# Kernel tuning notes

Hardware: AMD Instinct MI355X
Metric: run time of the kernel (lower is better)

Reference implementation:

```python
import jax, jax.numpy as jnp
import numpy as np

T, B, I, H = 4096, 2048, 1, 10


def setup_inputs() -> dict:
    key = jax.random.key(0)
    ks = jax.random.split(key, 8)
    k = 1.0 / np.sqrt(H)  # torch default init bound for RNN and Linear(10,1)
    u = lambda kk, shape: jax.random.uniform(kk, shape, jnp.float32, -k, k)
    return {
        "x": jax.random.normal(ks[0], (T, B, I), jnp.float32),
        "h": jnp.zeros((1, B, H), jnp.float32),
        "W_ih": u(ks[1], (H, I)),
        "b_ih": u(ks[2], (H,)),
        "W_hh": u(ks[3], (H, H)),
        "b_hh": u(ks[4], (H,)),
        "W_out": u(ks[5], (1, H)),
        "b_out": u(ks[6], (1,)),
    }


def reference(x, h, W_ih, b_ih, W_hh, b_hh, W_out, b_out):
    # Vanilla RNN: h_t = tanh(x_t @ W_ih^T + b_ih + h_{t-1} @ W_hh^T + b_hh)
    b = b_ih + b_hh  # fuse the two biases once

    def step(h_prev, x_t):  # h_prev: [B,H], x_t: [B,I]
        h_new = jnp.tanh(x_t @ W_ih.T + h_prev @ W_hh.T + b)
        return h_new, h_new

    h_last, ys = jax.lax.scan(step, h[0], x)  # ys: [T,B,H]
    out = ys @ W_out.T + b_out  # [T,B,1]
    return out, h_last[None]  # h: [1,B,H]
```

## Files before the change

kernel.cpp:

```cpp
#include <hip/hip_runtime.h>

#define T_STEPS 4096
#define BATCH   2048
#define HID     10
#define UB      16

__device__ __forceinline__ void issue16(float (&xr)[UB], const float* base) {
#pragma unroll
    for (int u = 0; u < UB; ++u)
        asm volatile("global_load_dword %0, %1, off"
                     : "=v"(xr[u]) : "v"(base + (size_t)u * BATCH) : "memory");
}
#define BIND16(a) "+v"(a[0]),"+v"(a[1]),"+v"(a[2]),"+v"(a[3]),"+v"(a[4]), \
    "+v"(a[5]),"+v"(a[6]),"+v"(a[7]),"+v"(a[8]),"+v"(a[9]),"+v"(a[10]),   \
    "+v"(a[11]),"+v"(a[12]),"+v"(a[13]),"+v"(a[14]),"+v"(a[15])
__device__ __forceinline__ void wait1_bind(float (&xr)[UB]) {
    asm volatile("s_waitcnt vmcnt(1)" : BIND16(xr) :: "memory");
}
__device__ __forceinline__ void wait0_bind(float (&xr)[UB]) {
    asm volatile("s_waitcnt vmcnt(0)" : BIND16(xr) :: "memory");
}

#define STEP_HEAD \
    "v_fma_f32 %[c0], %[wih2], %[x], %[bj2]\n\t"                                    \
    "v_fmac_f32 %[c0], %[r], %[w0]\n\t"                                             \
    "v_mul_f32_dpp %[c1], %[r], %[w1] row_ror:1 row_mask:0xf bank_mask:0xf\n\t"     \
    "v_mul_f32_dpp %[c2], %[r], %[w2] row_ror:2 row_mask:0xf bank_mask:0xf\n\t"     \
    "v_fmac_f32_dpp %[c0], %[r], %[w3] row_ror:3 row_mask:0xf bank_mask:0xf\n\t"    \
    "v_fmac_f32_dpp %[c1], %[r], %[w4] row_ror:4 row_mask:0xf bank_mask:0xf\n\t"    \
    "v_fmac_f32_dpp %[c2], %[r], %[w5] row_ror:5 row_mask:0xf bank_mask:0xf\n\t"    \
    "v_fmac_f32_dpp %[c0], %[r], %[w6] row_ror:6 row_mask:0xf bank_mask:0xf\n\t"    \
    "v_fmac_f32_dpp %[c1], %[r], %[w7] row_ror:7 row_mask:0xf bank_mask:0xf\n\t"    \
    "v_fmac_f32_dpp %[c2], %[r], %[w8] row_ror:8 row_mask:0xf bank_mask:0xf\n\t"    \
    "v_fmac_f32_dpp %[c0], %[r], %[w9] row_ror:9 row_mask:0xf bank_mask:0xf\n\t"    \
    "v_fmac_f32_dpp %[c1], %[r], %[w10] row_ror:10 row_mask:0xf bank_mask:0xf\n\t"  \
    "v_fmac_f32_dpp %[c2], %[r], %[w11] row_ror:11 row_mask:0xf bank_mask:0xf\n\t"  \
    "v_fmac_f32_dpp %[c0], %[r], %[w12] row_ror:12 row_mask:0xf bank_mask:0xf\n\t"  \
    "v_fmac_f32_dpp %[c1], %[r], %[w13] row_ror:13 row_mask:0xf bank_mask:0xf\n\t"  \
    "v_fmac_f32_dpp %[c2], %[r], %[w14] row_ror:14 row_mask:0xf bank_mask:0xf\n\t"  \
    "v_fmac_f32_dpp %[c0], %[r], %[w15] row_ror:15 row_mask:0xf bank_mask:0xf\n\t"  \
    "v_add_f32 %[c1], %[c1], %[c2]\n\t"                                             \
    "v_add_f32 %[c0], %[c0], %[c1]\n\t"                                             \
    "v_exp_f32 %[ex], %[c0]\n\t"                                                    \
    "s_nop 0\n\t"                                                                   \
    "v_add_f32 %[ex], 1.0, %[ex]\n\t"

#define STEP_TAIL \
    "v_rcp_f32 %[r], %[ex]\n\t"                                                     \
    "s_nop 0"

#define PKDPP(N) "v_fmac_f32_dpp %[pk], %[c0], %[m] row_ror:" #N " row_mask:0xf bank_mask:0xf\n\t"
#define PKPLAIN  "v_fmac_f32 %[pk], %[c0], %[m]\n\t"

#define DEF_STEP(SUF, PKLINE_) \
__device__ __forceinline__ void step_##SUF(float& r, float& pk, float x, \
        float wih2, float bj2, float m, const float (&w)[16]) { \
    float c0, c1, c2, ex; \
    asm volatile( STEP_HEAD PKLINE_ STEP_TAIL \
        : [c0]"=&v"(c0), [c1]"=&v"(c1), [c2]"=&v"(c2), [ex]"=&v"(ex), \
          [r]"+v"(r), [pk]"+v"(pk) \
        : [x]"v"(x), [wih2]"v"(wih2), [bj2]"v"(bj2), [m]"v"(m), \
          [w0]"v"(w[0]),  [w1]"v"(w[1]),  [w2]"v"(w[2]),  [w3]"v"(w[3]), \
          [w4]"v"(w[4]),  [w5]"v"(w[5]),  [w6]"v"(w[6]),  [w7]"v"(w[7]), \
          [w8]"v"(w[8]),  [w9]"v"(w[9]),  [w10]"v"(w[10]),[w11]"v"(w[11]), \
          [w12]"v"(w[12]),[w13]"v"(w[13]),[w14]"v"(w[14]),[w15]"v"(w[15])); \
}

DEF_STEP(r0,  PKPLAIN)
DEF_STEP(r1,  PKDPP(1))
DEF_STEP(r2,  PKDPP(2))
DEF_STEP(r3,  PKDPP(3))
DEF_STEP(r4,  PKDPP(4))
DEF_STEP(r6,  PKDPP(6))
DEF_STEP(r7,  PKDPP(7))
DEF_STEP(r8,  PKDPP(8))
DEF_STEP(r9,  PKDPP(9))
DEF_STEP(r10, PKDPP(10))
DEF_STEP(r11, PKDPP(11))
DEF_STEP(r12, PKDPP(12))
DEF_STEP(r13, PKDPP(13))
DEF_STEP(r14, PKDPP(14))
DEF_STEP(r15, PKDPP(15))

template<int U>
__device__ __forceinline__ void step_u(float& r, float& pk, float x,
                                       float wih2, float bj2,
                                       const float (&km)[16], float mz,
                                       const float (&w)[16]) {
    constexpr int ROT = (U + 5) & 15;
    float m;
    if constexpr (U == 0) m = mz; else m = km[U - 1];
    if constexpr (ROT == 0)       step_r0 (r, pk, x, wih2, bj2, m, w);
    else if constexpr (ROT == 1)  step_r1 (r, pk, x, wih2, bj2, m, w);
    else if constexpr (ROT == 2)  step_r2 (r, pk, x, wih2, bj2, m, w);
    else if constexpr (ROT == 3)  step_r3 (r, pk, x, wih2, bj2, m, w);
    else if constexpr (ROT == 4)  step_r4 (r, pk, x, wih2, bj2, m, w);
    else if constexpr (ROT == 6)  step_r6 (r, pk, x, wih2, bj2, m, w);
    else if constexpr (ROT == 7)  step_r7 (r, pk, x, wih2, bj2, m, w);
    else if constexpr (ROT == 8)  step_r8 (r, pk, x, wih2, bj2, m, w);
    else if constexpr (ROT == 9)  step_r9 (r, pk, x, wih2, bj2, m, w);
    else if constexpr (ROT == 10) step_r10(r, pk, x, wih2, bj2, m, w);
    else if constexpr (ROT == 11) step_r11(r, pk, x, wih2, bj2, m, w);
    else if constexpr (ROT == 12) step_r12(r, pk, x, wih2, bj2, m, w);
    else if constexpr (ROT == 13) step_r13(r, pk, x, wih2, bj2, m, w);
    else if constexpr (ROT == 14) step_r14(r, pk, x, wih2, bj2, m, w);
    else                          step_r15(r, pk, x, wih2, bj2, m, w);
}

template<int U>
__device__ __forceinline__ void run16(float& r, float& pk, const float (&xr)[UB],
                                      float wih2, float bj2,
                                      const float (&km)[16], float mz,
                                      const float (&w)[16]) {
    if constexpr (U < UB) {
        step_u<U>(r, pk, xr[U], wih2, bj2, km, mz, w);
        run16<U + 1>(r, pk, xr, wih2, bj2, km, mz, w);
    }
}

__device__ __forceinline__ void finish_reduce(float r, float& p, float& pk,
                                              float wo2, float m15) {
    asm volatile(
        "v_mul_f32 %[p], %[wo2], %[r]\n\t"
        "s_nop 1\n\t"
        "v_add_f32_dpp %[p], %[p], %[p] row_ror:8 row_mask:0xf bank_mask:0xf\n\t"
        "s_nop 1\n\t"
        "v_add_f32_dpp %[p], %[p], %[p] row_ror:4 row_mask:0xf bank_mask:0xf\n\t"
        "s_nop 1\n\t"
        "v_add_f32_dpp %[p], %[p], %[p] row_ror:2 row_mask:0xf bank_mask:0xf\n\t"
        "s_nop 1\n\t"
        "v_add_f32_dpp %[p], %[p], %[p] row_ror:1 row_mask:0xf bank_mask:0xf\n\t"
        "s_nop 1\n\t"
        "v_fmac_f32 %[pk], %[p], %[m]"
        : [p]"+v"(p), [pk]"+v"(pk)
        : [r]"v"(r), [wo2]"v"(wo2), [m]"v"(m15));
}

__global__ __launch_bounds__(64, 1) void rnn_kernel(
    const float* __restrict__ x,
    const float* __restrict__ h0,
    const float* __restrict__ W_ih,
    const float* __restrict__ b_ih,
    const float* __restrict__ W_hh,
    const float* __restrict__ b_hh,
    const float* __restrict__ W_out,
    const float* __restrict__ b_out,
    float* __restrict__ out)
{
    const int tid = threadIdx.x;
    const int j   = tid & 15;
    const int b   = (blockIdx.x << 2) + (tid >> 4);
    const bool jv = (j < HID);
    const int jc  = jv ? j : 0;

    const float CC = 2.88539008177792681472f;

    const float wih = jv ? W_ih[jc] : 0.0f;
    const float bj  = jv ? (b_ih[jc] + b_hh[jc]) : 0.0f;
    const float wo  = jv ? W_out[jc] : 0.0f;

    float wsh[16];
    float wsum = 0.0f;
#pragma unroll
    for (int N = 0; N < 16; ++N) {
        const int k = (j - N) & 15;
        wsh[N] = (jv && k < HID) ? W_hh[jc * HID + k] : 0.0f;
        wsum += wsh[N];
    }

    const float wih2 = CC * wih;
    const float bj2  = CC * (bj + wsum);
    float w2[16];
#pragma unroll
    for (int N = 0; N < 16; ++N) {
        if (jv) {
            w2[N] = -2.0f * CC * wsh[N];
        } else if (j == 10) {
            const int k = (10 - N) & 15;
            w2[N] = (k < HID) ? (-2.0f * W_out[k]) : 0.0f;
        } else {
            w2[N] = 0.0f;
        }
    }
    const float wo2 = -2.0f * wo;
    float c0sum = b_out[0];
#pragma unroll
    for (int k = 0; k < HID; ++k) c0sum += W_out[k];

    float km[16];
#pragma unroll
    for (int i = 0; i < 16; ++i) km[i] = (j == i) ? 1.0f : 0.0f;
    const float mzero = 0.0f;

    float rval = fmaf(-0.5f, jv ? h0[b * HID + jc] : 0.0f, 0.5f);
    float p = 0.0f, pk = 0.0f;

    const float* xb = x + b;
    float xA[UB], xB[UB];

    issue16(xA, xb);
    wait0_bind(xA);

    for (int t0 = 0; t0 < T_STEPS; t0 += 2 * UB) {
        wait1_bind(xA);
        issue16(xB, xb + (size_t)(t0 + UB) * BATCH);
        run16<0>(rval, pk, xA, wih2, bj2, km, mzero, w2);
        finish_reduce(rval, p, pk, wo2, km[15]);
        out[(size_t)(t0 + j) * BATCH + b] = pk + c0sum;
        pk = 0.0f;

        wait1_bind(xB);
        const float* xsrc = (t0 + 2 * UB < T_STEPS)
                          ? (xb + (size_t)(t0 + 2 * UB) * BATCH) : xb;
        issue16(xA, xsrc);
        run16<0>(rval, pk, xB, wih2, bj2, km, mzero, w2);
        finish_reduce(rval, p, pk, wo2, km[15]);
        out[(size_t)(t0 + UB + j) * BATCH + b] = pk + c0sum;
        pk = 0.0f;
    }

    wait0_bind(xA);

    if (jv) out[(size_t)T_STEPS * BATCH + (size_t)b * HID + j]
                = fmaf(-2.0f, rval, 1.0f);
}

extern "C" void kernel_launch(void* const* d_in, const int* in_sizes, int n_in,
                              void* d_out, int out_size, void* d_ws, size_t ws_size,
                              hipStream_t stream) {
    const float* x     = (const float*)d_in[0];
    const float* h0    = (const float*)d_in[1];
    const float* W_ih  = (const float*)d_in[2];
    const float* b_ih  = (const float*)d_in[3];
    const float* W_hh  = (const float*)d_in[4];
    const float* b_hh  = (const float*)d_in[5];
    const float* W_out = (const float*)d_in[6];
    const float* b_out = (const float*)d_in[7];

    rnn_kernel<<<BATCH / 4, 64, 0, stream>>>(
        x, h0, W_ih, b_ih, W_hh, b_hh, W_out, b_out, (float*)d_out);
}
```

Measured before the change: 331.1 us.

## Interleave two batch groups per wavefront to hide serial RNN step latency

```diff
diff --git a/kernel.cpp b/kernel.cpp
--- a/kernel.cpp
+++ b/kernel.cpp
@@ -20,120 +20,155 @@
 __device__ __forceinline__ void wait0_bind(float (&xr)[UB]) {
     asm volatile("s_waitcnt vmcnt(0)" : BIND16(xr) :: "memory");
 }
-
-#define STEP_HEAD \
-    "v_fma_f32 %[c0], %[wih2], %[x], %[bj2]\n\t"                                    \
-    "v_fmac_f32 %[c0], %[r], %[w0]\n\t"                                             \
-    "v_mul_f32_dpp %[c1], %[r], %[w1] row_ror:1 row_mask:0xf bank_mask:0xf\n\t"     \
-    "v_mul_f32_dpp %[c2], %[r], %[w2] row_ror:2 row_mask:0xf bank_mask:0xf\n\t"     \
-    "v_fmac_f32_dpp %[c0], %[r], %[w3] row_ror:3 row_mask:0xf bank_mask:0xf\n\t"    \
-    "v_fmac_f32_dpp %[c1], %[r], %[w4] row_ror:4 row_mask:0xf bank_mask:0xf\n\t"    \
-    "v_fmac_f32_dpp %[c2], %[r], %[w5] row_ror:5 row_mask:0xf bank_mask:0xf\n\t"    \
-    "v_fmac_f32_dpp %[c0], %[r], %[w6] row_ror:6 row_mask:0xf bank_mask:0xf\n\t"    \
-    "v_fmac_f32_dpp %[c1], %[r], %[w7] row_ror:7 row_mask:0xf bank_mask:0xf\n\t"    \
-    "v_fmac_f32_dpp %[c2], %[r], %[w8] row_ror:8 row_mask:0xf bank_mask:0xf\n\t"    \
-    "v_fmac_f32_dpp %[c0], %[r], %[w9] row_ror:9 row_mask:0xf bank_mask:0xf\n\t"    \
-    "v_fmac_f32_dpp %[c1], %[r], %[w10] row_ror:10 row_mask:0xf bank_mask:0xf\n\t"  \
-    "v_fmac_f32_dpp %[c2], %[r], %[w11] row_ror:11 row_mask:0xf bank_mask:0xf\n\t"  \
-    "v_fmac_f32_dpp %[c0], %[r], %[w12] row_ror:12 row_mask:0xf bank_mask:0xf\n\t"  \
-    "v_fmac_f32_dpp %[c1], %[r], %[w13] row_ror:13 row_mask:0xf bank_mask:0xf\n\t"  \
-    "v_fmac_f32_dpp %[c2], %[r], %[w14] row_ror:14 row_mask:0xf bank_mask:0xf\n\t"  \
-    "v_fmac_f32_dpp %[c0], %[r], %[w15] row_ror:15 row_mask:0xf bank_mask:0xf\n\t"  \
-    "v_add_f32 %[c1], %[c1], %[c2]\n\t"                                             \
-    "v_add_f32 %[c0], %[c0], %[c1]\n\t"                                             \
-    "v_exp_f32 %[ex], %[c0]\n\t"                                                    \
-    "s_nop 0\n\t"                                                                   \
-    "v_add_f32 %[ex], 1.0, %[ex]\n\t"
-
-#define STEP_TAIL \
-    "v_rcp_f32 %[r], %[ex]\n\t"                                                     \
-    "s_nop 0"
-
-#define PKDPP(N) "v_fmac_f32_dpp %[pk], %[c0], %[m] row_ror:" #N " row_mask:0xf bank_mask:0xf\n\t"
-#define PKPLAIN  "v_fmac_f32 %[pk], %[c0], %[m]\n\t"
-
-#define DEF_STEP(SUF, PKLINE_) \
-__device__ __forceinline__ void step_##SUF(float& r, float& pk, float x, \
+__device__ __forceinline__ void bind16(float (&xr)[UB]) {
+    asm volatile("" : BIND16(xr));
+}
+
+#define PKD(N) \
+    "v_fmac_f32_dpp %[pkA], %[c0A], %[m] row_ror:" #N " row_mask:0xf bank_mask:0xf\n\t" \
+    "v_fmac_f32_dpp %[pkB], %[c0B], %[m] row_ror:" #N " row_mask:0xf bank_mask:0xf\n\t"
+#define PKP \
+    "v_fmac_f32 %[pkA], %[c0A], %[m]\n\t" \
+    "v_fmac_f32 %[pkB], %[c0B], %[m]\n\t"
+
+#define DSTEP_BODY(PK_) \
+    "v_fma_f32 %[c0A], %[wih2], %[xA], %[bj2]\n\t"                                    \
+    "v_fma_f32 %[c0B], %[wih2], %[xB], %[bj2]\n\t"                                    \
+    "v_fmac_f32 %[c0A], %[rA], %[w0]\n\t"                                             \
+    "v_fmac_f32 %[c0B], %[rB], %[w0]\n\t"                                             \
+    "v_mul_f32_dpp %[c1A], %[rA], %[w1] row_ror:1 row_mask:0xf bank_mask:0xf\n\t"     \
+    "v_mul_f32_dpp %[c1B], %[rB], %[w1] row_ror:1 row_mask:0xf bank_mask:0xf\n\t"     \
+    "v_fmac_f32_dpp %[c1A], %[rA], %[w2] row_ror:2 row_mask:0xf bank_mask:0xf\n\t"    \
+    "v_fmac_f32_dpp %[c1B], %[rB], %[w2] row_ror:2 row_mask:0xf bank_mask:0xf\n\t"    \
+    "v_fmac_f32_dpp %[c1A], %[rA], %[w3] row_ror:3 row_mask:0xf bank_mask:0xf\n\t"    \
+    "v_fmac_f32_dpp %[c1B], %[rB], %[w3] row_ror:3 row_mask:0xf bank_mask:0xf\n\t"    \
+    "v_fmac_f32_dpp %[c1A], %[rA], %[w4] row_ror:4 row_mask:0xf bank_mask:0xf\n\t"    \
+    "v_fmac_f32_dpp %[c1B], %[rB], %[w4] row_ror:4 row_mask:0xf bank_mask:0xf\n\t"    \
+    "v_fmac_f32_dpp %[c1A], %[rA], %[w5] row_ror:5 row_mask:0xf bank_mask:0xf\n\t"    \
+    "v_fmac_f32_dpp %[c1B], %[rB], %[w5] row_ror:5 row_mask:0xf bank_mask:0xf\n\t"    \
+    "v_fmac_f32_dpp %[c1A], %[rA], %[w6] row_ror:6 row_mask:0xf bank_mask:0xf\n\t"    \
+    "v_fmac_f32_dpp %[c1B], %[rB], %[w6] row_ror:6 row_mask:0xf bank_mask:0xf\n\t"    \
+    "v_fmac_f32_dpp %[c1A], %[rA], %[w7] row_ror:7 row_mask:0xf bank_mask:0xf\n\t"    \
+    "v_fmac_f32_dpp %[c1B], %[rB], %[w7] row_ror:7 row_mask:0xf bank_mask:0xf\n\t"    \
+    "v_fmac_f32_dpp %[c1A], %[rA], %[w8] row_ror:8 row_mask:0xf bank_mask:0xf\n\t"    \
+    "v_fmac_f32_dpp %[c1B], %[rB], %[w8] row_ror:8 row_mask:0xf bank_mask:0xf\n\t"    \
+    "v_fmac_f32_dpp %[c1A], %[rA], %[w9] row_ror:9 row_mask:0xf bank_mask:0xf\n\t"    \
+    "v_fmac_f32_dpp %[c1B], %[rB], %[w9] row_ror:9 row_mask:0xf bank_mask:0xf\n\t"    \
+    "v_fmac_f32_dpp %[c1A], %[rA], %[w10] row_ror:10 row_mask:0xf bank_mask:0xf\n\t"  \
+    "v_fmac_f32_dpp %[c1B], %[rB], %[w10] row_ror:10 row_mask:0xf bank_mask:0xf\n\t"  \
+    "v_fmac_f32_dpp %[c0A], %[rA], %[w11] row_ror:11 row_mask:0xf bank_mask:0xf\n\t"  \
+    "v_fmac_f32_dpp %[c0B], %[rB], %[w11] row_ror:11 row_mask:0xf bank_mask:0xf\n\t"  \
+    "v_fmac_f32_dpp %[c0A], %[rA], %[w12] row_ror:12 row_mask:0xf bank_mask:0xf\n\t"  \
+    "v_fmac_f32_dpp %[c0B], %[rB], %[w12] row_ror:12 row_mask:0xf bank_mask:0xf\n\t"  \
+    "v_fmac_f32_dpp %[c0A], %[rA], %[w13] row_ror:13 row_mask:0xf bank_mask:0xf\n\t"  \
+    "v_fmac_f32_dpp %[c0B], %[rB], %[w13] row_ror:13 row_mask:0xf bank_mask:0xf\n\t"  \
+    "v_fmac_f32_dpp %[c0A], %[rA], %[w14] row_ror:14 row_mask:0xf bank_mask:0xf\n\t"  \
+    "v_fmac_f32_dpp %[c0B], %[rB], %[w14] row_ror:14 row_mask:0xf bank_mask:0xf\n\t"  \
+    "v_fmac_f32_dpp %[c0A], %[rA], %[w15] row_ror:15 row_mask:0xf bank_mask:0xf\n\t"  \
+    "v_fmac_f32_dpp %[c0B], %[rB], %[w15] row_ror:15 row_mask:0xf bank_mask:0xf\n\t"  \
+    "v_add_f32 %[c0A], %[c0A], %[c1A]\n\t"                                            \
+    "v_add_f32 %[c0B], %[c0B], %[c1B]\n\t"                                            \
+    "v_exp_f32 %[c1A], %[c0A]\n\t"                                                    \
+    "v_exp_f32 %[c1B], %[c0B]\n\t"                                                    \
+    PK_                                                                               \
+    "v_add_f32 %[c1A], 1.0, %[c1A]\n\t"                                               \
+    "v_add_f32 %[c1B], 1.0, %[c1B]\n\t"                                               \
+    "v_rcp_f32 %[rA], %[c1A]\n\t"                                                     \
+    "v_rcp_f32 %[rB], %[c1B]"
+
+#define DEF_DSTEP(SUF, PKLINE_) \
+__device__ __forceinline__ void dstep_##SUF(float& rA, float& rB, \
+        float& pkA, float& pkB, float xA, float xB, \
         float wih2, float bj2, float m, const float (&w)[16]) { \
-    float c0, c1, c2, ex; \
-    asm volatile( STEP_HEAD PKLINE_ STEP_TAIL \
-        : [c0]"=&v"(c0), [c1]"=&v"(c1), [c2]"=&v"(c2), [ex]"=&v"(ex), \
-          [r]"+v"(r), [pk]"+v"(pk) \
-        : [x]"v"(x), [wih2]"v"(wih2), [bj2]"v"(bj2), [m]"v"(m), \
+    float c0A, c1A, c0B, c1B; \
+    asm volatile( DSTEP_BODY(PKLINE_) \
+        : [c0A]"=&v"(c0A), [c1A]"=&v"(c1A), [c0B]"=&v"(c0B), [c1B]"=&v"(c1B), \
+          [rA]"+v"(rA), [rB]"+v"(rB), [pkA]"+v"(pkA), [pkB]"+v"(pkB) \
+        : [xA]"v"(xA), [xB]"v"(xB), [wih2]"v"(wih2), [bj2]"v"(bj2), [m]"v"(m), \
           [w0]"v"(w[0]),  [w1]"v"(w[1]),  [w2]"v"(w[2]),  [w3]"v"(w[3]), \
           [w4]"v"(w[4]),  [w5]"v"(w[5]),  [w6]"v"(w[6]),  [w7]"v"(w[7]), \
           [w8]"v"(w[8]),  [w9]"v"(w[9]),  [w10]"v"(w[10]),[w11]"v"(w[11]), \
           [w12]"v"(w[12]),[w13]"v"(w[13]),[w14]"v"(w[14]),[w15]"v"(w[15])); \
 }
 
-DEF_STEP(r0,  PKPLAIN)
-DEF_STEP(r1,  PKDPP(1))
-DEF_STEP(r2,  PKDPP(2))
-DEF_STEP(r3,  PKDPP(3))
-DEF_STEP(r4,  PKDPP(4))
-DEF_STEP(r6,  PKDPP(6))
-DEF_STEP(r7,  PKDPP(7))
-DEF_STEP(r8,  PKDPP(8))
-DEF_STEP(r9,  PKDPP(9))
-DEF_STEP(r10, PKDPP(10))
-DEF_STEP(r11, PKDPP(11))
-DEF_STEP(r12, PKDPP(12))
-DEF_STEP(r13, PKDPP(13))
-DEF_STEP(r14, PKDPP(14))
-DEF_STEP(r15, PKDPP(15))
+DEF_DSTEP(r0,  PKP)
+DEF_DSTEP(r1,  PKD(1))
+DEF_DSTEP(r2,  PKD(2))
+DEF_DSTEP(r3,  PKD(3))
+DEF_DSTEP(r4,  PKD(4))
+DEF_DSTEP(r5,  PKD(5))
+DEF_DSTEP(r6,  PKD(6))
+DEF_DSTEP(r7,  PKD(7))
+DEF_DSTEP(r8,  PKD(8))
+DEF_DSTEP(r9,  PKD(9))
+DEF_DSTEP(r10, PKD(10))
+DEF_DSTEP(r11, PKD(11))
+DEF_DSTEP(r12, PKD(12))
+DEF_DSTEP(r13, PKD(13))
+DEF_DSTEP(r14, PKD(14))
+DEF_DSTEP(r15, PKD(15))
 
 template<int U>
-__device__ __forceinline__ void step_u(float& r, float& pk, float x,
-                                       float wih2, float bj2,
-                                       const float (&km)[16], float mz,
-                                       const float (&w)[16]) {
+__device__ __forceinline__ void dstep_u(float& rA, float& rB, float& pkA, float& pkB,
+                                        float xA, float xB, float wih2, float bj2,
+                                        const float (&km)[16], float mz,
+                                        const float (&w)[16]) {
     constexpr int ROT = (U + 5) & 15;
     float m;
     if constexpr (U == 0) m = mz; else m = km[U - 1];
-    if constexpr (ROT == 0)       step_r0 (r, pk, x, wih2, bj2, m, w);
-    else if constexpr (ROT == 1)  step_r1 (r, pk, x, wih2, bj2, m, w);
-    else if constexpr (ROT == 2)  step_r2 (r, pk, x, wih2, bj2, m, w);
-    else if constexpr (ROT == 3)  step_r3 (r, pk, x, wih2, bj2, m, w);
-    else if constexpr (ROT == 4)  step_r4 (r, pk, x, wih2, bj2, m, w);
-    else if constexpr (ROT == 6)  step_r6 (r, pk, x, wih2, bj2, m, w);
-    else if constexpr (ROT == 7)  step_r7 (r, pk, x, wih2, bj2, m, w);
-    else if constexpr (ROT == 8)  step_r8 (r, pk, x, wih2, bj2, m, w);
-    else if constexpr (ROT == 9)  step_r9 (r, pk, x, wih2, bj2, m, w);
-    else if constexpr (ROT == 10) step_r10(r, pk, x, wih2, bj2, m, w);
-    else if constexpr (ROT == 11) step_r11(r, pk, x, wih2, bj2, m, w);
-    else if constexpr (ROT == 12) step_r12(r, pk, x, wih2, bj2, m, w);
-    else if constexpr (ROT == 13) step_r13(r, pk, x, wih2, bj2, m, w);
-    else if constexpr (ROT == 14) step_r14(r, pk, x, wih2, bj2, m, w);
-    else                          step_r15(r, pk, x, wih2, bj2, m, w);
+    if constexpr (ROT == 0)       dstep_r0 (rA, rB, pkA, pkB, xA, xB, wih2, bj2, m, w);
+    else if constexpr (ROT == 1)  dstep_r1 (rA, rB, pkA, pkB, xA, xB, wih2, bj2, m, w);
+    else if constexpr (ROT == 2)  dstep_r2 (rA, rB, pkA, pkB, xA, xB, wih2, bj2, m, w);
+    else if constexpr (ROT == 3)  dstep_r3 (rA, rB, pkA, pkB, xA, xB, wih2, bj2, m, w);
+    else if constexpr (ROT == 4)  dstep_r4 (rA, rB, pkA, pkB, xA, xB, wih2, bj2, m, w);
+    else if constexpr (ROT == 5)  dstep_r5 (rA, rB, pkA, pkB, xA, xB, wih2, bj2, m, w);
+    else if constexpr (ROT == 6)  dstep_r6 (rA, rB, pkA, pkB, xA, xB, wih2, bj2, m, w);
+    else if constexpr (ROT == 7)  dstep_r7 (rA, rB, pkA, pkB, xA, xB, wih2, bj2, m, w);
+    else if constexpr (ROT == 8)  dstep_r8 (rA, rB, pkA, pkB, xA, xB, wih2, bj2, m, w);
+    else if constexpr (ROT == 9)  dstep_r9 (rA, rB, pkA, pkB, xA, xB, wih2, bj2, m, w);
+    else if constexpr (ROT == 10) dstep_r10(rA, rB, pkA, pkB, xA, xB, wih2, bj2, m, w);
+    else if constexpr (ROT == 11) dstep_r11(rA, rB, pkA, pkB, xA, xB, wih2, bj2, m, w);
+    else if constexpr (ROT == 12) dstep_r12(rA, rB, pkA, pkB, xA, xB, wih2, bj2, m, w);
+    else if constexpr (ROT == 13) dstep_r13(rA, rB, pkA, pkB, xA, xB, wih2, bj2, m, w);
+    else if constexpr (ROT == 14) dstep_r14(rA, rB, pkA, pkB, xA, xB, wih2, bj2, m, w);
+    else                          dstep_r15(rA, rB, pkA, pkB, xA, xB, wih2, bj2, m, w);
 }
 
 template<int U>
-__device__ __forceinline__ void run16(float& r, float& pk, const float (&xr)[UB],
+__device__ __forceinline__ void run16(float& rA, float& rB, float& pkA, float& pkB,
+                                      const float (&xa)[UB], const float (&xb)[UB],
                                       float wih2, float bj2,
                                       const float (&km)[16], float mz,
                                       const float (&w)[16]) {
     if constexpr (U < UB) {
-        step_u<U>(r, pk, xr[U], wih2, bj2, km, mz, w);
-        run16<U + 1>(r, pk, xr, wih2, bj2, km, mz, w);
-    }
-}
-
-__device__ __forceinline__ void finish_reduce(float r, float& p, float& pk,
-                                              float wo2, float m15) {
+        dstep_u<U>(rA, rB, pkA, pkB, xa[U], xb[U], wih2, bj2, km, mz, w);
+        run16<U + 1>(rA, rB, pkA, pkB, xa, xb, wih2, bj2, km, mz, w);
+    }
+}
+
+__device__ __forceinline__ void finish2(float rA, float rB, float& pkA, float& pkB,
+                                        float wo2, float m15) {
+    float pA, pB;
     asm volatile(
-        "v_mul_f32 %[p], %[wo2], %[r]\n\t"
-        "s_nop 1\n\t"
-        "v_add_f32_dpp %[p], %[p], %[p] row_ror:8 row_mask:0xf bank_mask:0xf\n\t"
-        "s_nop 1\n\t"
-        "v_add_f32_dpp %[p], %[p], %[p] row_ror:4 row_mask:0xf bank_mask:0xf\n\t"
-        "s_nop 1\n\t"
-        "v_add_f32_dpp %[p], %[p], %[p] row_ror:2 row_mask:0xf bank_mask:0xf\n\t"
-        "s_nop 1\n\t"
-        "v_add_f32_dpp %[p], %[p], %[p] row_ror:1 row_mask:0xf bank_mask:0xf\n\t"
-        "s_nop 1\n\t"
-        "v_fmac_f32 %[pk], %[p], %[m]"
-        : [p]"+v"(p), [pk]"+v"(pk)
-        : [r]"v"(r), [wo2]"v"(wo2), [m]"v"(m15));
+        "v_mul_f32 %[pA], %[wo2], %[rA]\n\t"
+        "v_mul_f32 %[pB], %[wo2], %[rB]\n\t"
+        "s_nop 0\n\t"
+        "v_add_f32_dpp %[pA], %[pA], %[pA] row_ror:8 row_mask:0xf bank_mask:0xf\n\t"
+        "v_add_f32_dpp %[pB], %[pB], %[pB] row_ror:8 row_mask:0xf bank_mask:0xf\n\t"
+        "s_nop 0\n\t"
+        "v_add_f32_dpp %[pA], %[pA], %[pA] row_ror:4 row_mask:0xf bank_mask:0xf\n\t"
+        "v_add_f32_dpp %[pB], %[pB], %[pB] row_ror:4 row_mask:0xf bank_mask:0xf\n\t"
+        "s_nop 0\n\t"
+        "v_add_f32_dpp %[pA], %[pA], %[pA] row_ror:2 row_mask:0xf bank_mask:0xf\n\t"
+        "v_add_f32_dpp %[pB], %[pB], %[pB] row_ror:2 row_mask:0xf bank_mask:0xf\n\t"
+        "s_nop 0\n\t"
+        "v_add_f32_dpp %[pA], %[pA], %[pA] row_ror:1 row_mask:0xf bank_mask:0xf\n\t"
+        "v_add_f32_dpp %[pB], %[pB], %[pB] row_ror:1 row_mask:0xf bank_mask:0xf\n\t"
+        "s_nop 0\n\t"
+        "v_fmac_f32 %[pkA], %[pA], %[m]\n\t"
+        "v_fmac_f32 %[pkB], %[pB], %[m]"
+        : [pA]"=&v"(pA), [pB]"=&v"(pB), [pkA]"+v"(pkA), [pkB]"+v"(pkB)
+        : [rA]"v"(rA), [rB]"v"(rB), [wo2]"v"(wo2), [m]"v"(m15));
 }
 
 __global__ __launch_bounds__(64, 1) void rnn_kernel(
@@ -149,7 +184,8 @@
 {
     const int tid = threadIdx.x;
     const int j   = tid & 15;
-    const int b   = (blockIdx.x << 2) + (tid >> 4);
+    const int bA  = (blockIdx.x << 3) + (tid >> 4);
+    const int bB  = bA + 4;
     const bool jv = (j < HID);
     const int jc  = jv ? j : 0;
 
@@ -192,37 +228,45 @@
     for (int i = 0; i < 16; ++i) km[i] = (j == i) ? 1.0f : 0.0f;
     const float mzero = 0.0f;
 
-    float rval = fmaf(-0.5f, jv ? h0[b * HID + jc] : 0.0f, 0.5f);
-    float p = 0.0f, pk = 0.0f;
-
-    const float* xb = x + b;
-    float xA[UB], xB[UB];
-
-    issue16(xA, xb);
-    wait0_bind(xA);
+    float rA = fmaf(-0.5f, jv ? h0[bA * HID + jc] : 0.0f, 0.5f);
+    float rB = fmaf(-0.5f, jv ? h0[bB * HID + jc] : 0.0f, 0.5f);
+    float pkA = 0.0f, pkB = 0.0f;
+
+    const float* xbA = x + bA;
+    const float* xbB = x + bB;
+    float axA[UB], axB[UB], bxA[UB], bxB[UB];
+
+    issue16(axA, xbA);
+    issue16(axB, xbB);
+    wait0_bind(axA); bind16(axB);
 
     for (int t0 = 0; t0 < T_STEPS; t0 += 2 * UB) {
-        wait1_bind(xA);
-        issue16(xB, xb + (size_t)(t0 + UB) * BATCH);
-        run16<0>(rval, pk, xA, wih2, bj2, km, mzero, w2);
-        finish_reduce(rval, p, pk, wo2, km[15]);
-        out[(size_t)(t0 + j) * BATCH + b] = pk + c0sum;
-        pk = 0.0f;
-
-        wait1_bind(xB);
-        const float* xsrc = (t0 + 2 * UB < T_STEPS)
-                          ? (xb + (size_t)(t0 + 2 * UB) * BATCH) : xb;
-        issue16(xA, xsrc);
-        run16<0>(rval, pk, xB, wih2, bj2, km, mzero, w2);
-        finish_reduce(rval, p, pk, wo2, km[15]);
-        out[(size_t)(t0 + UB + j) * BATCH + b] = pk + c0sum;
-        pk = 0.0f;
-    }
-
-    wait0_bind(xA);
-
-    if (jv) out[(size_t)T_STEPS * BATCH + (size_t)b * HID + j]
-                = fmaf(-2.0f, rval, 1.0f);
+        wait1_bind(axA); bind16(axB);
+        issue16(bxA, xbA + (size_t)(t0 + UB) * BATCH);
+        issue16(bxB, xbB + (size_t)(t0 + UB) * BATCH);
+        run16<0>(rA, rB, pkA, pkB, axA, axB, wih2, bj2, km, mzero, w2);
+        finish2(rA, rB, pkA, pkB, wo2, km[15]);
+        out[(size_t)(t0 + j) * BATCH + bA] = pkA + c0sum;
+        out[(size_t)(t0 + j) * BATCH + bB] = pkB + c0sum;
+        pkA = 0.0f; pkB = 0.0f;
+
+        wait1_bind(bxA); bind16(bxB);
+        const bool more = (t0 + 2 * UB < T_STEPS);
+        issue16(axA, more ? (xbA + (size_t)(t0 + 2 * UB) * BATCH) : xbA);
+        issue16(axB, more ? (xbB + (size_t)(t0 + 2 * UB) * BATCH) : xbB);
+        run16<0>(rA, rB, pkA, pkB, bxA, bxB, wih2, bj2, km, mzero, w2);
+        finish2(rA, rB, pkA, pkB, wo2, km[15]);
+        out[(size_t)(t0 + UB + j) * BATCH + bA] = pkA + c0sum;
+        out[(size_t)(t0 + UB + j) * BATCH + bB] = pkB + c0sum;
+        pkA = 0.0f; pkB = 0.0f;
+    }
+
+    wait0_bind(axA); bind16(axB);
+
+    if (jv) {
+        out[(size_t)T_STEPS * BATCH + (size_t)bA * HID + j] = fmaf(-2.0f, rA, 1.0f);
+        out[(size_t)T_STEPS * BATCH + (size_t)bB * HID + j] = fmaf(-2.0f, rB, 1.0f);
+    }
 }
 
 extern "C" void kernel_launch(void* const* d_in, const int* in_sizes, int n_in,
@@ -237,6 +281,6 @@
     const float* W_out = (const float*)d_in[6];
     const float* b_out = (const float*)d_in[7];
 
-    rnn_kernel<<<BATCH / 4, 64, 0, stream>>>(
+    rnn_kernel<<<BATCH / 8, 64, 0, stream>>>(
         x, h0, W_ih, b_ih, W_hh, b_hh, W_out, b_out, (float*)d_out);
 }
```

Result: slower. 550.3 us (+66.2%).
